# Kernel tuning notes

Measured on AMD Instinct MI355X. Metric: run time of the kernel, lower is better.

Reference implementation:

```python
import jax, jax.numpy as jnp
import numpy as np

BS, L, NPH, NQ, H = 64, 512, 16, 16, 1024
EPS = 1e-5

def _ln(x, g, b):
    m = jnp.mean(x, axis=-1, keepdims=True)
    v = jnp.mean((x - m) ** 2, axis=-1, keepdims=True)
    return (x - m) * jax.lax.rsqrt(v + EPS) * g + b

def setup_inputs() -> dict:
    key = jax.random.key(0)
    ks = jax.random.split(key, 24)
    s = 0.02
    inp = {
        "lang_context_feat": jax.random.normal(ks[0], (BS, L, H), jnp.float32),
        "lang_query_feat": jax.random.normal(ks[1], (BS, NPH, H), jnp.float32),
        "mask_query_context": jax.random.randint(ks[2], (BS, NPH, L), 0, 2).astype(bool),
        "query_embed": jax.random.normal(ks[3], (NQ, 2 * H), jnp.float32) * s,
        # linear1/2/3: hidden -> hidden (stored [in, out])
        "W1": jax.random.normal(ks[4], (H, H), jnp.float32) * s, "b1": jnp.zeros((H,), jnp.float32),
        "W2": jax.random.normal(ks[5], (H, H), jnp.float32) * s, "b2": jnp.zeros((H,), jnp.float32),
        "W3": jax.random.normal(ks[6], (H, H), jnp.float32) * s, "b3": jnp.zeros((H,), jnp.float32),
        # context_out: Linear(h,h) + LayerNorm(h)
        "Wc": jax.random.normal(ks[7], (H, H), jnp.float32) * s, "bc": jnp.zeros((H,), jnp.float32),
        "gc": jnp.ones((H,), jnp.float32), "betac": jnp.zeros((H,), jnp.float32),
        # fuse_encoder_query: Linear(2h,h)+LN+ReLU+Dropout(eval)+Linear(h,h)+LN+ReLU
        "Wf1": jax.random.normal(ks[8], (2 * H, H), jnp.float32) * s, "bf1": jnp.zeros((H,), jnp.float32),
        "gf1": jnp.ones((H,), jnp.float32), "betaf1": jnp.zeros((H,), jnp.float32),
        "Wf2": jax.random.normal(ks[9], (H, H), jnp.float32) * s, "bf2": jnp.zeros((H,), jnp.float32),
        "gf2": jnp.ones((H,), jnp.float32), "betaf2": jnp.zeros((H,), jnp.float32),
    }
    return inp

def reference(lang_context_feat, lang_query_feat, mask_query_context,
              query_embed, W1, b1, W2, b2, W3, b3,
              Wc, bc, gc, betac,
              Wf1, bf1, gf1, betaf1, Wf2, bf2, gf2, betaf2):
    # single-query attention: k from first context token, q/v from all tokens
    k = lang_context_feat[:, 0:1, :] @ W1 + b1          # [bs,1,h]
    q = lang_context_feat @ W2 + b2                     # [bs,L,h]
    v = lang_context_feat @ W3 + b3                     # [bs,L,h]
    att = jnp.einsum("bih,blh->bil", k, q)             # [bs,1,L]
    att = jnp.broadcast_to(att, mask_query_context.shape)  # [bs,n_ph,L]
    att = jnp.where(mask_query_context, -jnp.inf, att)
    p = jax.nn.softmax(att, axis=-1)                    # [bs,n_ph,L]
    ctx = jnp.einsum("bpl,blh->bph", p, v)             # [bs,n_ph,h]
    ctx = _ln(ctx @ Wc + bc, gc, betac)
    ctx = lang_context_feat[:, None, 0, :] + ctx        # residual with first token
    x = jnp.concatenate([ctx, lang_query_feat], axis=-1)   # [bs,n_ph,2h]
    x = jax.nn.relu(_ln(x @ Wf1 + bf1, gf1, betaf1))        # dropout: eval mode (identity)
    x = jax.nn.relu(_ln(x @ Wf2 + bf2, gf2, betaf2))        # [bs,n_ph,h]
    # repeat(1,1,1,2) on last dim == tile [x, x]
    pq = jnp.concatenate([x, x], axis=-1)[:, :, None, :]    # [bs,n_ph,1,2h]
    pq = pq + query_embed[None, None, :, :]                 # [bs,n_ph,n_q,2h]
    pq = pq.reshape(pq.shape[0], -1, 2 * H).transpose(1, 0, 2)  # [n_ph*n_q,bs,2h]
    return pq[..., :H], pq[..., H:]
```

## Files before the change

kernel.cpp:

```cpp
#include <hip/hip_runtime.h>

typedef __bf16 bf16;
typedef __bf16 bf16x8 __attribute__((ext_vector_type(8)));
typedef __bf16 bf16x4 __attribute__((ext_vector_type(4)));
typedef float f32x4 __attribute__((ext_vector_type(4)));

#define LCTX 512
#define HD 1024

__device__ __forceinline__ float wave_sum(float v) {
    for (int off = 32; off; off >>= 1) v += __shfl_xor(v, off, 64);
    return v;
}
__device__ __forceinline__ float wave_max(float v) {
    for (int off = 32; off; off >>= 1) v = fmaxf(v, __shfl_xor(v, off, 64));
    return v;
}

__global__ __launch_bounds__(256) void prep_kernel(const float* __restrict__ W3,
                                                   const float* __restrict__ Wc,
                                                   const float* __restrict__ Wf1,
                                                   const float* __restrict__ Wf2,
                                                   const float* __restrict__ lq,
                                                   const float* __restrict__ x,
                                                   const float* __restrict__ W1,
                                                   bf16* __restrict__ W3t, bf16* __restrict__ Wct,
                                                   bf16* __restrict__ Wf1t, bf16* __restrict__ Wf2t,
                                                   bf16* __restrict__ X,
                                                   float* __restrict__ kpartial) {
    __shared__ __align__(16) char smem[33792];
    int blk = blockIdx.x, t = threadIdx.x;
    if (blk < 5120) {
        float (*tile)[33] = (float(*)[33])smem;
        const float* W; bf16* Wt; int K, N, i;
        if (blk < 1024)      { W = W3;  Wt = W3t;  K = 1024; N = 1024; i = blk; }
        else if (blk < 2048) { W = Wc;  Wt = Wct;  K = 1024; N = 1024; i = blk - 1024; }
        else if (blk < 3072) { W = Wf2; Wt = Wf2t; K = 1024; N = 1024; i = blk - 2048; }
        else                 { W = Wf1; Wt = Wf1t; K = 2048; N = 1024; i = blk - 3072; }
        int k0 = (i >> 5) * 32, n0 = (i & 31) * 32;
        int c = t & 31, r = t >> 5;
#pragma unroll
        for (int j = 0; j < 4; j++)
            tile[r + j * 8][c] = W[(size_t)(k0 + r + j * 8) * N + n0 + c];
        __syncthreads();
#pragma unroll
        for (int j = 0; j < 4; j++)
            Wt[(size_t)(n0 + r + j * 8) * K + k0 + c] = (bf16)tile[c][r + j * 8];
    } else if (blk < 6144) {
        int i = (blk - 5120) * 256 + t;
        float4 v = ((const float4*)lq)[i];
        int row = i >> 8, h4 = i & 255;
        bf16x4 o = {(bf16)v.x, (bf16)v.y, (bf16)v.z, (bf16)v.w};
        *(bf16x4*)(X + (size_t)row * 2048 + 1024 + h4 * 4) = o;
    } else {
        float (*xs)[68] = (float(*)[68])smem;
        float (*wsm)[64] = (float(*)[64])(smem + 17408);
        int kv = blk - 6144;
        int n0 = (kv & 15) * 64, k0 = (kv >> 4) * 64;
#pragma unroll
        for (int i = 0; i < 4; i++) {
            int f = t + i * 256;
            int b = f >> 4, c = f & 15;
            *(float4*)&xs[b][c * 4] =
                *(const float4*)(x + (size_t)b * LCTX * HD + k0 + c * 4);
        }
#pragma unroll
        for (int i = 0; i < 4; i++) {
            int f = t + i * 256;
            int r = f >> 4, c = f & 15;
            *(float4*)&wsm[r][c * 4] =
                *(const float4*)(W1 + (size_t)(k0 + r) * 1024 + n0 + c * 4);
        }
        __syncthreads();
        int tb = t >> 4, tc = t & 15;
        int b0 = tb * 4;
        float acc[4][4] = {};
        for (int kk = 0; kk < 64; kk += 4) {
            float4 w0 = *(const float4*)&wsm[kk + 0][tc * 4];
            float4 w1 = *(const float4*)&wsm[kk + 1][tc * 4];
            float4 w2 = *(const float4*)&wsm[kk + 2][tc * 4];
            float4 w3 = *(const float4*)&wsm[kk + 3][tc * 4];
            float4 xv[4];
#pragma unroll
            for (int bi = 0; bi < 4; bi++) xv[bi] = *(const float4*)&xs[b0 + bi][kk];
#pragma unroll
            for (int bi = 0; bi < 4; bi++) {
                acc[bi][0] += xv[bi].x * w0.x + xv[bi].y * w1.x + xv[bi].z * w2.x + xv[bi].w * w3.x;
                acc[bi][1] += xv[bi].x * w0.y + xv[bi].y * w1.y + xv[bi].z * w2.y + xv[bi].w * w3.y;
                acc[bi][2] += xv[bi].x * w0.z + xv[bi].y * w1.z + xv[bi].z * w2.z + xv[bi].w * w3.z;
                acc[bi][3] += xv[bi].x * w0.w + xv[bi].y * w1.w + xv[bi].z * w2.w + xv[bi].w * w3.w;
            }
        }
        float* pout = kpartial + ((size_t)(kv >> 4) * 64 + b0) * 1024 + n0 + tc * 4;
#pragma unroll
        for (int bi = 0; bi < 4; bi++)
            *(float4*)(pout + (size_t)bi * 1024) =
                make_float4(acc[bi][0], acc[bi][1], acc[bi][2], acc[bi][3]);
    }
}

__global__ __launch_bounds__(256) void mmat_kernel(const float* __restrict__ partial,
                                                   const float* __restrict__ b1,
                                                   const float* __restrict__ W2,
                                                   float* __restrict__ mout) {
    __shared__ float ks[1024];
    int b = blockIdx.x, i0 = blockIdx.y * 64, t = threadIdx.x;
    {
        float4 acc = ((const float4*)b1)[t];
#pragma unroll
        for (int kt = 0; kt < 16; kt++) {
            float4 v = ((const float4*)(partial + ((size_t)kt * 64 + b) * 1024))[t];
            acc.x += v.x; acc.y += v.y; acc.z += v.z; acc.w += v.w;
        }
        *(float4*)&ks[t * 4] = acc;
    }
    __syncthreads();
    int wave = t >> 6, lane = t & 63;
    for (int rr = 0; rr < 16; rr++) {
        int i = i0 + wave * 16 + rr;
        const float* wrow = W2 + (size_t)i * 1024;
        float s = 0.f;
#pragma unroll
        for (int j = 0; j < 4; j++) {
            float4 wv = ((const float4*)wrow)[lane + j * 64];
            const float4 kv = *(const float4*)&ks[(lane + j * 64) * 4];
            s += wv.x * kv.x + wv.y * kv.y + wv.z * kv.z + wv.w * kv.w;
        }
        s = wave_sum(s);
        if (lane == 0) mout[(size_t)b * 1024 + i] = s;
    }
}

__global__ __launch_bounds__(256) void att_kernel(const float* __restrict__ x,
                                                  const float* __restrict__ m,
                                                  float* __restrict__ att) {
    __shared__ float ms[1024];
    int b = blockIdx.x, l0 = blockIdx.y * 32, t = threadIdx.x;
    *(float4*)&ms[t * 4] = ((const float4*)(m + (size_t)b * 1024))[t];
    __syncthreads();
    int wave = t >> 6, lane = t & 63;
    for (int rr = 0; rr < 8; rr++) {
        int l = l0 + wave * 8 + rr;
        const float* xr = x + ((size_t)b * LCTX + l) * HD;
        float s = 0.f;
#pragma unroll
        for (int j = 0; j < 4; j++) {
            float4 xv = ((const float4*)xr)[lane + j * 64];
            const float4 mv = *(const float4*)&ms[(lane + j * 64) * 4];
            s += xv.x * mv.x + xv.y * mv.y + xv.z * mv.z + xv.w * mv.w;
        }
        s = wave_sum(s);
        if (lane == 0) att[(size_t)b * LCTX + l] = s;
    }
}

__global__ __launch_bounds__(256) void ypart_kernel(const float* __restrict__ att,
                                                    const unsigned char* __restrict__ mask,
                                                    const float* __restrict__ x,
                                                    float* __restrict__ ypartial) {
    __shared__ float ps[16][64];
    __shared__ float att_s[512];
    __shared__ int sstr;
    int b = blockIdx.x, lqi = blockIdx.y, t = threadIdx.x;
    int l0 = lqi * 64;
    int wave = t >> 6, lane = t & 63;
    if (t == 0) sstr = 4;
    if (t < 128) ((float4*)att_s)[t] = ((const float4*)(att + (size_t)b * LCTX))[t];
    __syncthreads();
    if (t < 128 && ((const unsigned int*)mask)[t] > 1u) sstr = 1;
    __syncthreads();
    int stride = sstr;
#pragma unroll
    for (int q = 0; q < 4; q++) {
        int pp = wave * 4 + q;
        size_t mbase = ((size_t)(b * 16 + pp)) * LCTX;
        float av[8];
#pragma unroll
        for (int j = 0; j < 8; j++) {
            int l = lane + j * 64;
            bool mk = mask[(mbase + l) * (size_t)stride] != 0;
            av[j] = mk ? -1e30f : att_s[l];
        }
        float mx = av[0];
#pragma unroll
        for (int j = 1; j < 8; j++) mx = fmaxf(mx, av[j]);
        mx = wave_max(mx);
        float s = 0.f;
#pragma unroll
        for (int j = 0; j < 8; j++) {
            av[j] = (av[j] <= -1e29f) ? 0.f : expf(av[j] - mx);
            s += av[j];
        }
        s = wave_sum(s);
        float sel = av[0];
#pragma unroll
        for (int j = 1; j < 8; j++) if (lqi == j) sel = av[j];
        ps[pp][lane] = sel * (1.f / s);
    }
    __syncthreads();
    float4 acc[16];
#pragma unroll
    for (int q = 0; q < 16; q++) acc[q] = make_float4(0.f, 0.f, 0.f, 0.f);
    const float4* xb = (const float4*)(x + ((size_t)b * LCTX + l0) * HD) + t;
    float4 xv = xb[0];
    for (int l = 0; l < 64; l++) {
        float4 cur = xv;
        if (l < 63) xv = xb[(size_t)(l + 1) * 256];
#pragma unroll
        for (int q = 0; q < 16; q++) {
            float pv = ps[q][l];
            acc[q].x += pv * cur.x; acc[q].y += pv * cur.y;
            acc[q].z += pv * cur.z; acc[q].w += pv * cur.w;
        }
    }
    float* yp = ypartial + ((size_t)lqi * 1024 + b * 16) * 1024 + t * 4;
#pragma unroll
    for (int q = 0; q < 16; q++)
        *(float4*)(yp + (size_t)q * 1024) = acc[q];
}

__global__ __launch_bounds__(256) void yred_kernel(const float* __restrict__ ypartial,
                                                   bf16* __restrict__ y) {
    int i = blockIdx.x * 256 + threadIdx.x;
    float4 s = ((const float4*)ypartial)[i];
#pragma unroll
    for (int c = 1; c < 8; c++) {
        float4 v = ((const float4*)(ypartial + (size_t)c * 1024 * 1024))[i];
        s.x += v.x; s.y += v.y; s.z += v.z; s.w += v.w;
    }
    bf16x4 o = {(bf16)s.x, (bf16)s.y, (bf16)s.z, (bf16)s.w};
    *(bf16x4*)(y + (size_t)i * 4) = o;
}

__device__ __forceinline__ void gl16(const bf16* g, bf16* l) {
    __builtin_amdgcn_global_load_lds((const __attribute__((address_space(1))) void*)g,
                                     (__attribute__((address_space(3))) void*)l, 16, 0, 0);
}
__device__ __forceinline__ bf16x8 ldsfrag(const bf16* base, int row, int kb) {
    return *(const bf16x8*)(base + row * 64 + ((kb ^ (row & 7)) << 3));
}

template <bool OUT_BF16>
__global__ __launch_bounds__(256) void gemm_kernel(const bf16* __restrict__ A, int lda,
                                                   const bf16* __restrict__ Bt, int ldb,
                                                   const float* __restrict__ bias,
                                                   void* __restrict__ Cv, int ldc, int K) {
    __shared__ bf16 sA[2][4096];
    __shared__ bf16 sB[2][2048];
    int tid = threadIdx.x;
    int wave = tid >> 6, lane = tid & 63;
    int m0 = blockIdx.x * 64, n0 = blockIdx.y * 32;
    int wr = wave * 16;
    int l16 = lane & 15, lhi = lane >> 4;
    int r0 = tid >> 3, kb = tid & 7;
    int r1 = r0 + 32;
    int sk0 = (kb ^ (r0 & 7)) << 3;
    int sk1 = (kb ^ (r1 & 7)) << 3;
    const bf16* A0 = A + (size_t)(m0 + r0) * lda + sk0;
    const bf16* A1 = A + (size_t)(m0 + r1) * lda + sk1;
    const bf16* B0 = Bt + (size_t)(n0 + r0) * ldb + sk0;
    int wbA0 = wave * 512, wbA1 = 2048 + wave * 512, wbB = wave * 512;

    f32x4 acc0 = {}, acc1 = {};

    int nt = K >> 6;
    gl16(A0, &sA[0][wbA0]); gl16(A1, &sA[0][wbA1]);
    gl16(B0, &sB[0][wbB]);
    asm volatile("s_waitcnt vmcnt(0)" ::: "memory");
    __syncthreads();
    int cur = 0;
    for (int tI = 0; tI < nt; ++tI) {
        if (tI + 1 < nt) {
            int ko = (tI + 1) << 6;
            gl16(A0 + ko, &sA[cur ^ 1][wbA0]); gl16(A1 + ko, &sA[cur ^ 1][wbA1]);
            gl16(B0 + ko, &sB[cur ^ 1][wbB]);
        }
        const bf16* a = sA[cur];
        const bf16* bt = sB[cur];
#pragma unroll
        for (int ks = 0; ks < 2; ks++) {
            int kbb = ks * 4 + lhi;
            bf16x8 av = ldsfrag(a, wr + l16, kbb);
            bf16x8 b0v = ldsfrag(bt, l16, kbb);
            bf16x8 b1v = ldsfrag(bt, 16 + l16, kbb);
            acc0 = __builtin_amdgcn_mfma_f32_16x16x32_bf16(av, b0v, acc0, 0, 0, 0);
            acc1 = __builtin_amdgcn_mfma_f32_16x16x32_bf16(av, b1v, acc1, 0, 0, 0);
        }
        asm volatile("s_waitcnt vmcnt(0)" ::: "memory");
        __syncthreads();
        cur ^= 1;
    }
    f32x4 accs[2] = {acc0, acc1};
#pragma unroll
    for (int ni = 0; ni < 2; ni++)
#pragma unroll
        for (int r = 0; r < 4; r++) {
            int row = m0 + wr + lhi * 4 + r;
            int col = n0 + ni * 16 + l16;
            float v = accs[ni][r] + bias[col];
            if (OUT_BF16)
                ((bf16*)Cv)[(size_t)row * ldc + col] = (bf16)v;
            else
                ((float*)Cv)[(size_t)row * ldc + col] = v;
        }
}

template <int MODE>
__global__ __launch_bounds__(256) void ln_kernel(const float* __restrict__ C,
                                                 const float* __restrict__ g,
                                                 const float* __restrict__ beta,
                                                 const float* __restrict__ resid,
                                                 void* __restrict__ out) {
    __shared__ float r1[8], r2[8];
    int row = blockIdx.x, t = threadIdx.x;
    float4 v = ((const float4*)(C + (size_t)row * 1024))[t];
    float s = v.x + v.y + v.z + v.w;
    float s2 = v.x * v.x + v.y * v.y + v.z * v.z + v.w * v.w;
    s = wave_sum(s); s2 = wave_sum(s2);
    int wave = t >> 6, lane = t & 63;
    if (lane == 0) { r1[wave] = s; r2[wave] = s2; }
    __syncthreads();
    float S = r1[0] + r1[1] + r1[2] + r1[3];
    float S2 = r2[0] + r2[1] + r2[2] + r2[3];
    float mean = S * (1.f / 1024.f);
    float var = S2 * (1.f / 1024.f) - mean * mean;
    float inv = rsqrtf(var + 1e-5f);
    float4 gv = ((const float4*)g)[t];
    float4 bv = ((const float4*)beta)[t];
    float o[4];
    o[0] = (v.x - mean) * inv * gv.x + bv.x;
    o[1] = (v.y - mean) * inv * gv.y + bv.y;
    o[2] = (v.z - mean) * inv * gv.z + bv.z;
    o[3] = (v.w - mean) * inv * gv.w + bv.w;
    if (MODE == 0) {
        int b = row >> 4;
        const float* x0 = resid + (size_t)b * LCTX * HD + t * 4;
        bf16x4 w = {(bf16)(o[0] + x0[0]), (bf16)(o[1] + x0[1]),
                    (bf16)(o[2] + x0[2]), (bf16)(o[3] + x0[3])};
        *(bf16x4*)((bf16*)out + (size_t)row * 2048 + t * 4) = w;
    } else {
        bf16x4 w = {(bf16)fmaxf(o[0], 0.f), (bf16)fmaxf(o[1], 0.f),
                    (bf16)fmaxf(o[2], 0.f), (bf16)fmaxf(o[3], 0.f)};
        *(bf16x4*)((bf16*)out + (size_t)row * 1024 + t * 4) = w;
    }
}

__global__ __launch_bounds__(256) void lnout_kernel(const float* __restrict__ C,
                                                    const float* __restrict__ g,
                                                    const float* __restrict__ beta,
                                                    const float* __restrict__ qe,
                                                    float* __restrict__ out) {
    __shared__ float r1[8], r2[8];
    int row = blockIdx.x, t = threadIdx.x;
    int b = row >> 4, pp = row & 15;
    float4 v = ((const float4*)(C + (size_t)row * 1024))[t];
    float s = v.x + v.y + v.z + v.w;
    float s2 = v.x * v.x + v.y * v.y + v.z * v.z + v.w * v.w;
    s = wave_sum(s); s2 = wave_sum(s2);
    int wave = t >> 6, lane = t & 63;
    if (lane == 0) { r1[wave] = s; r2[wave] = s2; }
    __syncthreads();
    float S = r1[0] + r1[1] + r1[2] + r1[3];
    float S2 = r2[0] + r2[1] + r2[2] + r2[3];
    float mean = S * (1.f / 1024.f);
    float var = S2 * (1.f / 1024.f) - mean * mean;
    float inv = rsqrtf(var + 1e-5f);
    float4 gv = ((const float4*)g)[t];
    float4 bv = ((const float4*)beta)[t];
    float4 ov;
    ov.x = fmaxf((v.x - mean) * inv * gv.x + bv.x, 0.f);
    ov.y = fmaxf((v.y - mean) * inv * gv.y + bv.y, 0.f);
    ov.z = fmaxf((v.z - mean) * inv * gv.z + bv.z, 0.f);
    ov.w = fmaxf((v.w - mean) * inv * gv.w + bv.w, 0.f);
    float* out0 = out;
    float* out1 = out + (size_t)256 * 64 * 1024;
#pragma unroll
    for (int q = 0; q < 16; q++) {
        float4 q0 = ((const float4*)(qe + (size_t)q * 2048))[t];
        float4 q1 = ((const float4*)(qe + (size_t)q * 2048 + 1024))[t];
        size_t orow = ((size_t)(pp * 16 + q) * 64 + b) * 1024;
        ((float4*)(out0 + orow))[t] =
            make_float4(ov.x + q0.x, ov.y + q0.y, ov.z + q0.z, ov.w + q0.w);
        ((float4*)(out1 + orow))[t] =
            make_float4(ov.x + q1.x, ov.y + q1.y, ov.z + q1.z, ov.w + q1.w);
    }
}

extern "C" void kernel_launch(void* const* d_in, const int* in_sizes, int n_in,
                              void* d_out, int out_size, void* d_ws, size_t ws_size,
                              hipStream_t stream) {
    const float* x      = (const float*)d_in[0];
    const float* lq     = (const float*)d_in[1];
    const unsigned char* mask = (const unsigned char*)d_in[2];
    const float* qe     = (const float*)d_in[3];
    const float* W1     = (const float*)d_in[4];
    const float* b1     = (const float*)d_in[5];
    const float* W2     = (const float*)d_in[6];
    const float* W3     = (const float*)d_in[8];
    const float* b3     = (const float*)d_in[9];
    const float* Wc     = (const float*)d_in[10];
    const float* bc     = (const float*)d_in[11];
    const float* gc     = (const float*)d_in[12];
    const float* betac  = (const float*)d_in[13];
    const float* Wf1    = (const float*)d_in[14];
    const float* bf1    = (const float*)d_in[15];
    const float* gf1    = (const float*)d_in[16];
    const float* betaf1 = (const float*)d_in[17];
    const float* Wf2    = (const float*)d_in[18];
    const float* bf2    = (const float*)d_in[19];
    const float* gf2    = (const float*)d_in[20];
    const float* betaf2 = (const float*)d_in[21];

    char* ws = (char*)d_ws;
    const size_t MB = 1 << 20;
    bf16* W3t   = (bf16*)(ws + 0 * MB);
    bf16* Wct   = (bf16*)(ws + 2 * MB);
    bf16* Wf1t  = (bf16*)(ws + 4 * MB);
    bf16* Wf2t  = (bf16*)(ws + 8 * MB);
    bf16* X     = (bf16*)(ws + 10 * MB);
    float* mbuf = (float*)(ws + 14 * MB + 256 * 1024);
    float* attb = (float*)(ws + 14 * MB + 512 * 1024);
    bf16* ybuf  = (bf16*)(ws + 17 * MB);
    bf16* ctxp  = (bf16*)(ws + 19 * MB);
    float* Cbuf = (float*)(ws + 21 * MB);
    bf16* t1    = (bf16*)(ws + 25 * MB);
    float* ypartial = (float*)(ws + 32 * MB);
    float* kpartial = Cbuf;

    prep_kernel<<<6400, 256, 0, stream>>>(W3, Wc, Wf1, Wf2, lq, x, W1,
                                          W3t, Wct, Wf1t, Wf2t, X, kpartial);
    mmat_kernel<<<dim3(64, 16), 256, 0, stream>>>(kpartial, b1, W2, mbuf);
    att_kernel<<<dim3(64, 16), 256, 0, stream>>>(x, mbuf, attb);
    ypart_kernel<<<dim3(64, 8), 256, 0, stream>>>(attb, mask, x, ypartial);
    yred_kernel<<<1024, 256, 0, stream>>>(ypartial, ybuf);
    gemm_kernel<true><<<dim3(16, 32), 256, 0, stream>>>(ybuf, 1024, W3t, 1024, b3,
                                                        ctxp, 1024, 1024);
    gemm_kernel<false><<<dim3(16, 32), 256, 0, stream>>>(ctxp, 1024, Wct, 1024, bc,
                                                         Cbuf, 1024, 1024);
    ln_kernel<0><<<1024, 256, 0, stream>>>(Cbuf, gc, betac, x, X);
    gemm_kernel<false><<<dim3(16, 32), 256, 0, stream>>>(X, 2048, Wf1t, 2048, bf1,
                                                         Cbuf, 1024, 2048);
    ln_kernel<1><<<1024, 256, 0, stream>>>(Cbuf, gf1, betaf1, nullptr, t1);
    gemm_kernel<false><<<dim3(16, 32), 256, 0, stream>>>(t1, 1024, Wf2t, 1024, bf2,
                                                         Cbuf, 1024, 1024);
    lnout_kernel<<<1024, 256, 0, stream>>>(Cbuf, gf2, betaf2, qe, (float*)d_out);
}
```

Before: 230.1 us.

## Fuse y-reduction into ypart via last-block atomics; shrink GEMM and att tiles

Removes the separate yred kernel. Each batch's last-finishing ypart block, found with an atomic counter that prep_kernel zeroes, sums the eight partials and writes the bf16 y. GEMM tiles shrink from 64x32 to 32x32 with each wave owning a 16x16 subtile, which doubles the grid to 1024 blocks for better CU occupancy on the small M=1024 GEMMs. The att kernel also uses twice as many blocks with fewer rows each. In exchange, each GEMM block does less reuse per B load, and the fused reduction adds a fence and atomic per block.

Result: slower. 298.8 us (+29.9%).

```diff
diff --git a/kernel.cpp b/kernel.cpp
--- a/kernel.cpp
+++ b/kernel.cpp
@@ -27,7 +27,8 @@
                                                    bf16* __restrict__ W3t, bf16* __restrict__ Wct,
                                                    bf16* __restrict__ Wf1t, bf16* __restrict__ Wf2t,
                                                    bf16* __restrict__ X,
-                                                   float* __restrict__ kpartial) {
+                                                   float* __restrict__ kpartial,
+                                                   int* __restrict__ ycnt) {
     __shared__ __align__(16) char smem[33792];
     int blk = blockIdx.x, t = threadIdx.x;
     if (blk < 5120) {
@@ -52,7 +53,7 @@
         int row = i >> 8, h4 = i & 255;
         bf16x4 o = {(bf16)v.x, (bf16)v.y, (bf16)v.z, (bf16)v.w};
         *(bf16x4*)(X + (size_t)row * 2048 + 1024 + h4 * 4) = o;
-    } else {
+    } else if (blk < 6400) {
         float (*xs)[68] = (float(*)[68])smem;
         float (*wsm)[64] = (float(*)[64])(smem + 17408);
         int kv = blk - 6144;
@@ -96,6 +97,8 @@
         for (int bi = 0; bi < 4; bi++)
             *(float4*)(pout + (size_t)bi * 1024) =
                 make_float4(acc[bi][0], acc[bi][1], acc[bi][2], acc[bi][3]);
+    } else {
+        if (t < 64) ycnt[t] = 0;
     }
 }
 
@@ -135,12 +138,12 @@
                                                   const float* __restrict__ m,
                                                   float* __restrict__ att) {
     __shared__ float ms[1024];
-    int b = blockIdx.x, l0 = blockIdx.y * 32, t = threadIdx.x;
+    int b = blockIdx.x, l0 = blockIdx.y * 16, t = threadIdx.x;
     *(float4*)&ms[t * 4] = ((const float4*)(m + (size_t)b * 1024))[t];
     __syncthreads();
     int wave = t >> 6, lane = t & 63;
-    for (int rr = 0; rr < 8; rr++) {
-        int l = l0 + wave * 8 + rr;
+    for (int rr = 0; rr < 4; rr++) {
+        int l = l0 + wave * 4 + rr;
         const float* xr = x + ((size_t)b * LCTX + l) * HD;
         float s = 0.f;
 #pragma unroll
@@ -157,10 +160,13 @@
 __global__ __launch_bounds__(256) void ypart_kernel(const float* __restrict__ att,
                                                     const unsigned char* __restrict__ mask,
                                                     const float* __restrict__ x,
-                                                    float* __restrict__ ypartial) {
+                                                    float* __restrict__ ypartial,
+                                                    int* __restrict__ ycnt,
+                                                    bf16* __restrict__ y) {
     __shared__ float ps[16][64];
     __shared__ float att_s[512];
     __shared__ int sstr;
+    __shared__ int lastflag;
     int b = blockIdx.x, lqi = blockIdx.y, t = threadIdx.x;
     int l0 = lqi * 64;
     int wave = t >> 6, lane = t & 63;
@@ -217,19 +223,24 @@
 #pragma unroll
     for (int q = 0; q < 16; q++)
         *(float4*)(yp + (size_t)q * 1024) = acc[q];
-}
-
-__global__ __launch_bounds__(256) void yred_kernel(const float* __restrict__ ypartial,
-                                                   bf16* __restrict__ y) {
-    int i = blockIdx.x * 256 + threadIdx.x;
-    float4 s = ((const float4*)ypartial)[i];
-#pragma unroll
-    for (int c = 1; c < 8; c++) {
-        float4 v = ((const float4*)(ypartial + (size_t)c * 1024 * 1024))[i];
-        s.x += v.x; s.y += v.y; s.z += v.z; s.w += v.w;
-    }
-    bf16x4 o = {(bf16)s.x, (bf16)s.y, (bf16)s.z, (bf16)s.w};
-    *(bf16x4*)(y + (size_t)i * 4) = o;
+
+    __threadfence();
+    if (t == 0) lastflag = (atomicAdd(&ycnt[b], 1) == 7);
+    __syncthreads();
+    if (!lastflag) return;
+    __threadfence();
+    for (int i = t; i < 4096; i += 256) {
+        int pp = i >> 8, c4 = i & 255;
+        size_t base4 = ((size_t)b * 16 + pp) * 256 + c4;
+        float4 s = ((const float4*)ypartial)[base4];
+#pragma unroll
+        for (int c = 1; c < 8; c++) {
+            float4 v = ((const float4*)ypartial)[(size_t)c * 262144 + base4];
+            s.x += v.x; s.y += v.y; s.z += v.z; s.w += v.w;
+        }
+        bf16x4 o = {(bf16)s.x, (bf16)s.y, (bf16)s.z, (bf16)s.w};
+        *(bf16x4*)(y + (((size_t)b * 16 + pp) * 1024 + c4 * 4)) = o;
+    }
 }
 
 __device__ __forceinline__ void gl16(const bf16* g, bf16* l) {
@@ -245,35 +256,32 @@
                                                    const bf16* __restrict__ Bt, int ldb,
                                                    const float* __restrict__ bias,
                                                    void* __restrict__ Cv, int ldc, int K) {
-    __shared__ bf16 sA[2][4096];
+    __shared__ bf16 sA[2][2048];
     __shared__ bf16 sB[2][2048];
     int tid = threadIdx.x;
     int wave = tid >> 6, lane = tid & 63;
-    int m0 = blockIdx.x * 64, n0 = blockIdx.y * 32;
-    int wr = wave * 16;
+    int m0 = blockIdx.x * 32, n0 = blockIdx.y * 32;
+    int wr = (wave >> 1) * 16, wc = (wave & 1) * 16;
     int l16 = lane & 15, lhi = lane >> 4;
     int r0 = tid >> 3, kb = tid & 7;
-    int r1 = r0 + 32;
     int sk0 = (kb ^ (r0 & 7)) << 3;
-    int sk1 = (kb ^ (r1 & 7)) << 3;
     const bf16* A0 = A + (size_t)(m0 + r0) * lda + sk0;
-    const bf16* A1 = A + (size_t)(m0 + r1) * lda + sk1;
     const bf16* B0 = Bt + (size_t)(n0 + r0) * ldb + sk0;
-    int wbA0 = wave * 512, wbA1 = 2048 + wave * 512, wbB = wave * 512;
-
-    f32x4 acc0 = {}, acc1 = {};
+    int wb = wave * 512;
+
+    f32x4 acc = {};
 
     int nt = K >> 6;
-    gl16(A0, &sA[0][wbA0]); gl16(A1, &sA[0][wbA1]);
-    gl16(B0, &sB[0][wbB]);
+    gl16(A0, &sA[0][wb]);
+    gl16(B0, &sB[0][wb]);
     asm volatile("s_waitcnt vmcnt(0)" ::: "memory");
     __syncthreads();
     int cur = 0;
     for (int tI = 0; tI < nt; ++tI) {
         if (tI + 1 < nt) {
             int ko = (tI + 1) << 6;
-            gl16(A0 + ko, &sA[cur ^ 1][wbA0]); gl16(A1 + ko, &sA[cur ^ 1][wbA1]);
-            gl16(B0 + ko, &sB[cur ^ 1][wbB]);
+            gl16(A0 + ko, &sA[cur ^ 1][wb]);
+            gl16(B0 + ko, &sB[cur ^ 1][wb]);
         }
         const bf16* a = sA[cur];
         const bf16* bt = sB[cur];
@@ -281,28 +289,23 @@
         for (int ks = 0; ks < 2; ks++) {
             int kbb = ks * 4 + lhi;
             bf16x8 av = ldsfrag(a, wr + l16, kbb);
-            bf16x8 b0v = ldsfrag(bt, l16, kbb);
-            bf16x8 b1v = ldsfrag(bt, 16 + l16, kbb);
-            acc0 = __builtin_amdgcn_mfma_f32_16x16x32_bf16(av, b0v, acc0, 0, 0, 0);
-            acc1 = __builtin_amdgcn_mfma_f32_16x16x32_bf16(av, b1v, acc1, 0, 0, 0);
+            bf16x8 bv = ldsfrag(bt, wc + l16, kbb);
+            acc = __builtin_amdgcn_mfma_f32_16x16x32_bf16(av, bv, acc, 0, 0, 0);
         }
         asm volatile("s_waitcnt vmcnt(0)" ::: "memory");
         __syncthreads();
         cur ^= 1;
     }
-    f32x4 accs[2] = {acc0, acc1};
-#pragma unroll
-    for (int ni = 0; ni < 2; ni++)
-#pragma unroll
-        for (int r = 0; r < 4; r++) {
-            int row = m0 + wr + lhi * 4 + r;
-            int col = n0 + ni * 16 + l16;
-            float v = accs[ni][r] + bias[col];
-            if (OUT_BF16)
-                ((bf16*)Cv)[(size_t)row * ldc + col] = (bf16)v;
-            else
-                ((float*)Cv)[(size_t)row * ldc + col] = v;
-        }
+#pragma unroll
+    for (int r = 0; r < 4; r++) {
+        int row = m0 + wr + lhi * 4 + r;
+        int col = n0 + wc + l16;
+        float v = acc[r] + bias[col];
+        if (OUT_BF16)
+            ((bf16*)Cv)[(size_t)row * ldc + col] = (bf16)v;
+        else
+            ((float*)Cv)[(size_t)row * ldc + col] = v;
+    }
 }
 
 template <int MODE>
@@ -420,6 +423,7 @@
     bf16* X     = (bf16*)(ws + 10 * MB);
     float* mbuf = (float*)(ws + 14 * MB + 256 * 1024);
     float* attb = (float*)(ws + 14 * MB + 512 * 1024);
+    int* ycnt   = (int*)(ws + 15 * MB);
     bf16* ybuf  = (bf16*)(ws + 17 * MB);
     bf16* ctxp  = (bf16*)(ws + 19 * MB);
     float* Cbuf = (float*)(ws + 21 * MB);
@@ -427,21 +431,20 @@
     float* ypartial = (float*)(ws + 32 * MB);
     float* kpartial = Cbuf;
 
-    prep_kernel<<<6400, 256, 0, stream>>>(W3, Wc, Wf1, Wf2, lq, x, W1,
-                                          W3t, Wct, Wf1t, Wf2t, X, kpartial);
+    prep_kernel<<<6401, 256, 0, stream>>>(W3, Wc, Wf1, Wf2, lq, x, W1,
+                                          W3t, Wct, Wf1t, Wf2t, X, kpartial, ycnt);
     mmat_kernel<<<dim3(64, 16), 256, 0, stream>>>(kpartial, b1, W2, mbuf);
-    att_kernel<<<dim3(64, 16), 256, 0, stream>>>(x, mbuf, attb);
-    ypart_kernel<<<dim3(64, 8), 256, 0, stream>>>(attb, mask, x, ypartial);
-    yred_kernel<<<1024, 256, 0, stream>>>(ypartial, ybuf);
-    gemm_kernel<true><<<dim3(16, 32), 256, 0, stream>>>(ybuf, 1024, W3t, 1024, b3,
+    att_kernel<<<dim3(64, 32), 256, 0, stream>>>(x, mbuf, attb);
+    ypart_kernel<<<dim3(64, 8), 256, 0, stream>>>(attb, mask, x, ypartial, ycnt, ybuf);
+    gemm_kernel<true><<<dim3(32, 32), 256, 0, stream>>>(ybuf, 1024, W3t, 1024, b3,
                                                         ctxp, 1024, 1024);
-    gemm_kernel<false><<<dim3(16, 32), 256, 0, stream>>>(ctxp, 1024, Wct, 1024, bc,
+    gemm_kernel<false><<<dim3(32, 32), 256, 0, stream>>>(ctxp, 1024, Wct, 1024, bc,
                                                          Cbuf, 1024, 1024);
     ln_kernel<0><<<1024, 256, 0, stream>>>(Cbuf, gc, betac, x, X);
-    gemm_kernel<false><<<dim3(16, 32), 256, 0, stream>>>(X, 2048, Wf1t, 2048, bf1,
+    gemm_kernel<false><<<dim3(32, 32), 256, 0, stream>>>(X, 2048, Wf1t, 2048, bf1,
                                                          Cbuf, 1024, 2048);
     ln_kernel<1><<<1024, 256, 0, stream>>>(Cbuf, gf1, betaf1, nullptr, t1);
-    gemm_kernel<false><<<dim3(16, 32), 256, 0, stream>>>(t1, 1024, Wf2t, 1024, bf2,
+    gemm_kernel<false><<<dim3(32, 32), 256, 0, stream>>>(t1, 1024, Wf2t, 1024, bf2,
                                                          Cbuf, 1024, 1024);
     lnout_kernel<<<1024, 256, 0, stream>>>(Cbuf, gf2, betaf2, qe, (float*)d_out);
 }
```
